# Performance work log

Measured on AMD Instinct MI355X. Metric: run time of the kernel, lower is better.

Reference implementation:

```python
import jax, jax.numpy as jnp
import numpy as np

B, M, I = 32, 8192, 256
TEMPERATURE = 1.0


def setup_inputs() -> dict:
    key = jax.random.key(0)
    k1, k2, k3, k4 = jax.random.split(key, 4)
    memory = jax.random.normal(k1, (B, M, I), dtype=jnp.float32)
    qkey = jax.random.normal(k2, (B, I), dtype=jnp.float32)
    beta = jax.random.uniform(k3, (B,), dtype=jnp.float32)
    # xavier-uniform init for Linear(I, I)
    limit = float(np.sqrt(6.0 / (I + I)))
    W = jax.random.uniform(k4, (I, I), dtype=jnp.float32, minval=-limit, maxval=limit)
    b = jnp.zeros((I,), dtype=jnp.float32)
    return {"memory": memory, "key": qkey, "beta": beta, "W": W, "b": b}


def reference(memory, key, beta, W, b):
    # projected_key = tanh(key @ W^T + b)  -- torch Linear stores weight [out, in]
    projected_key = jnp.tanh(key @ W.T + b)                      # [B, I]
    diff = projected_key[:, None, :] - memory                    # [B, M, I]
    distances = jnp.sum(diff * diff, axis=-1)                    # [B, M]
    similarity = -distances
    weights = jax.nn.softmax(beta[:, None] * similarity / TEMPERATURE, axis=-1)  # [B, M]
    read_vector = jnp.einsum('bm,bmi->bi', weights, memory)      # [B, I]
    return weights, read_vector, similarity
```

## Files before the change

### kernel.cpp

```cpp
#include <hip/hip_runtime.h>
#include <math.h>

constexpr int Bdim = 32;
constexpr int Mdim = 8192;
constexpr int Idim = 256;
constexpr int ROWS_PER_BLOCK = 128;
constexpr int ROWS_PER_WAVE = 32;
constexpr int NCHUNK = Mdim / ROWS_PER_BLOCK;
constexpr int NSLICE = 8;

__global__ void proj_key_kernel(const float* __restrict__ key,
                                const float* __restrict__ W,
                                const float* __restrict__ bias,
                                float* __restrict__ pk) {
    int b = blockIdx.x;
    int i = threadIdx.x;
    __shared__ float kq[Idim];
    kq[i] = key[b * Idim + i];
    __syncthreads();
    const float4* w4 = (const float4*)(W + (size_t)i * Idim);
    const float4* k4 = (const float4*)kq;
    float s = bias[i];
    #pragma unroll 4
    for (int k = 0; k < Idim / 4; ++k) {
        float4 wv = w4[k];
        float4 kv = k4[k];
        s += wv.x * kv.x + wv.y * kv.y + wv.z * kv.z + wv.w * kv.w;
    }
    pk[b * Idim + i] = tanhf(s);
}

__global__ void fused_pass1_kernel(const float* __restrict__ memory,
                                   const float* __restrict__ pk,
                                   const float* __restrict__ beta,
                                   float* __restrict__ sim,
                                   float* __restrict__ pvec,
                                   float* __restrict__ pmx,
                                   float* __restrict__ psum) {
    int b = blockIdx.x / NCHUNK;
    int c = blockIdx.x % NCHUNK;
    int wave = threadIdx.x >> 6;
    int lane = threadIdx.x & 63;
    float bt = beta[b];

    float4 pkv = ((const float4*)(pk + b * Idim))[lane];

    int row0 = c * ROWS_PER_BLOCK + wave * ROWS_PER_WAVE;
    const float* base = memory + ((size_t)b * Mdim + row0) * Idim;
    float* simp = sim + (size_t)b * Mdim + row0;

    float mx = -INFINITY, ssum = 0.f;
    float4 acc = make_float4(0.f, 0.f, 0.f, 0.f);
    float my_sim = 0.f;

    auto body = [&](float4 mv, int r) {
        float dx = pkv.x - mv.x, dy = pkv.y - mv.y;
        float dz = pkv.z - mv.z, dw = pkv.w - mv.w;
        float s = dx * dx + dy * dy + dz * dz + dw * dw;
        #pragma unroll
        for (int off = 32; off; off >>= 1) s += __shfl_xor(s, off, 64);
        if (lane == r) my_sim = -s;
        float a = -bt * s;
        if (a > mx) {
            float sc = __expf(mx - a);
            ssum *= sc;
            acc.x *= sc; acc.y *= sc; acc.z *= sc; acc.w *= sc;
            mx = a;
        }
        float p = __expf(a - mx);
        ssum += p;
        acc.x = fmaf(p, mv.x, acc.x);
        acc.y = fmaf(p, mv.y, acc.y);
        acc.z = fmaf(p, mv.z, acc.z);
        acc.w = fmaf(p, mv.w, acc.w);
    };

    const float4* rp = (const float4*)base + lane;
    float4 cur = rp[0];
    float4 nxt = rp[64];
    #pragma unroll 2
    for (int r = 0; r < ROWS_PER_WAVE - 2; ++r) {
        float4 pf = rp[(size_t)(r + 2) * 64];
        body(cur, r);
        cur = nxt;
        nxt = pf;
    }
    body(cur, ROWS_PER_WAVE - 2);
    body(nxt, ROWS_PER_WAVE - 1);

    if (lane < 32) simp[lane] = my_sim;

    __shared__ float lacc[4][Idim];
    __shared__ float lmx[4], lsum[4];
    ((float4*)lacc[wave])[lane] = acc;
    if (lane == 0) { lmx[wave] = mx; lsum[wave] = ssum; }
    __syncthreads();

    float MX = fmaxf(fmaxf(lmx[0], lmx[1]), fmaxf(lmx[2], lmx[3]));
    float e0 = __expf(lmx[0] - MX), e1 = __expf(lmx[1] - MX);
    float e2 = __expf(lmx[2] - MX), e3 = __expf(lmx[3] - MX);
    int i = threadIdx.x;
    float v = lacc[0][i] * e0 + lacc[1][i] * e1 + lacc[2][i] * e2 + lacc[3][i] * e3;
    size_t pc = (size_t)b * NCHUNK + c;
    pvec[pc * Idim + i] = v;
    if (threadIdx.x == 0) {
        pmx[pc] = MX;
        psum[pc] = lsum[0] * e0 + lsum[1] * e1 + lsum[2] * e2 + lsum[3] * e3;
    }
}

__global__ void epilogue_kernel(const float* __restrict__ pvec,
                                const float* __restrict__ pmx,
                                const float* __restrict__ psum,
                                const float* __restrict__ sim,
                                const float* __restrict__ beta,
                                float* __restrict__ read_vec,
                                float* __restrict__ weights) {
    int b = blockIdx.x / NSLICE;
    int slice = blockIdx.x % NSLICE;
    int tid = threadIdx.x;
    __shared__ float e[NCHUNK];
    __shared__ float MXs, sInvs;

    if (tid < NCHUNK) {
        float m = pmx[(size_t)b * NCHUNK + tid];
        float mm = m;
        #pragma unroll
        for (int off = 32; off; off >>= 1) mm = fmaxf(mm, __shfl_xor(mm, off, 64));
        float ec = __expf(m - mm);
        e[tid] = ec;
        float sc = psum[(size_t)b * NCHUNK + tid] * ec;
        #pragma unroll
        for (int off = 32; off; off >>= 1) sc += __shfl_xor(sc, off, 64);
        if (tid == 0) { MXs = mm; sInvs = 1.f / sc; }
    }
    __syncthreads();

    float MX = MXs, inv = sInvs;

    if (slice == 0) {
        float v = 0.f;
        const float* p = pvec + (size_t)b * NCHUNK * Idim + tid;
        #pragma unroll 8
        for (int c = 0; c < NCHUNK; ++c) v += p[(size_t)c * Idim] * e[c];
        read_vec[(size_t)b * Idim + tid] = v * inv;
    }

    float bt = beta[b];
    int m4 = slice * (Mdim / NSLICE / 4) + tid;
    float4 s = ((const float4*)(sim + (size_t)b * Mdim))[m4];
    float4 w;
    w.x = __expf(bt * s.x - MX) * inv;
    w.y = __expf(bt * s.y - MX) * inv;
    w.z = __expf(bt * s.z - MX) * inv;
    w.w = __expf(bt * s.w - MX) * inv;
    ((float4*)(weights + (size_t)b * Mdim))[m4] = w;
}

extern "C" void kernel_launch(void* const* d_in, const int* in_sizes, int n_in,
                              void* d_out, int out_size, void* d_ws, size_t ws_size,
                              hipStream_t stream) {
    const float* memory = (const float*)d_in[0];
    const float* key    = (const float*)d_in[1];
    const float* beta   = (const float*)d_in[2];
    const float* W      = (const float*)d_in[3];
    const float* bias   = (const float*)d_in[4];

    float* out = (float*)d_out;
    float* weights  = out;
    float* read_vec = out + (size_t)Bdim * Mdim;
    float* sim      = read_vec + (size_t)Bdim * Idim;

    float* pk   = (float*)d_ws;
    float* pvec = pk + (size_t)Bdim * Idim;
    float* pmx  = pvec + (size_t)Bdim * NCHUNK * Idim;
    float* psum = pmx + (size_t)Bdim * NCHUNK;

    proj_key_kernel<<<Bdim, Idim, 0, stream>>>(key, W, bias, pk);
    fused_pass1_kernel<<<Bdim * NCHUNK, 256, 0, stream>>>(memory, pk, beta,
                                                          sim, pvec, pmx, psum);
    epilogue_kernel<<<Bdim * NSLICE, 256, 0, stream>>>(pvec, pmx, psum, sim, beta,
                                                       read_vec, weights);
}
```

Baseline: 62.35 us.

## Batch eight rows per online-softmax step and split projection across more blocks

The main pass now loads eight memory rows at once, does their eight butterfly reductions interleaved, and updates the running max once per group instead of once per row. This exposes more memory-level and shuffle-level parallelism and cuts serial rescale branches. The projection kernel is also split over 8x more blocks, with 8 lanes cooperating on each output row via shuffles, so it uses more of the GPU. Register pressure rises from holding eight float4 rows.

```diff
diff --git a/kernel.cpp b/kernel.cpp
--- a/kernel.cpp
+++ b/kernel.cpp
@@ -13,21 +13,25 @@
                                 const float* __restrict__ W,
                                 const float* __restrict__ bias,
                                 float* __restrict__ pk) {
-    int b = blockIdx.x;
-    int i = threadIdx.x;
-    __shared__ float kq[Idim];
-    kq[i] = key[b * Idim + i];
-    __syncthreads();
-    const float4* w4 = (const float4*)(W + (size_t)i * Idim);
-    const float4* k4 = (const float4*)kq;
-    float s = bias[i];
-    #pragma unroll 4
-    for (int k = 0; k < Idim / 4; ++k) {
+    int b = blockIdx.x >> 3;
+    int slice = blockIdx.x & 7;
+    int tid = threadIdx.x;
+    int row = slice * 32 + (tid >> 3);
+    int seg = tid & 7;
+
+    const float4* w4 = (const float4*)(W + (size_t)row * Idim) + seg * 8;
+    const float4* k4 = (const float4*)(key + (size_t)b * Idim) + seg * 8;
+    float s = 0.f;
+    #pragma unroll
+    for (int k = 0; k < 8; ++k) {
         float4 wv = w4[k];
         float4 kv = k4[k];
         s += wv.x * kv.x + wv.y * kv.y + wv.z * kv.z + wv.w * kv.w;
     }
-    pk[b * Idim + i] = tanhf(s);
+    s += __shfl_xor(s, 4, 64);
+    s += __shfl_xor(s, 2, 64);
+    s += __shfl_xor(s, 1, 64);
+    if (seg == 0) pk[(size_t)b * Idim + row] = tanhf(s + bias[row]);
 }
 
 __global__ void fused_pass1_kernel(const float* __restrict__ memory,
@@ -43,7 +47,7 @@
     int lane = threadIdx.x & 63;
     float bt = beta[b];
 
-    float4 pkv = ((const float4*)(pk + b * Idim))[lane];
+    float4 pkv = ((const float4*)(pk + (size_t)b * Idim))[lane];
 
     int row0 = c * ROWS_PER_BLOCK + wave * ROWS_PER_WAVE;
     const float* base = memory + ((size_t)b * Mdim + row0) * Idim;
@@ -53,41 +57,50 @@
     float4 acc = make_float4(0.f, 0.f, 0.f, 0.f);
     float my_sim = 0.f;
 
-    auto body = [&](float4 mv, int r) {
-        float dx = pkv.x - mv.x, dy = pkv.y - mv.y;
-        float dz = pkv.z - mv.z, dw = pkv.w - mv.w;
-        float s = dx * dx + dy * dy + dz * dz + dw * dw;
+    const float4* rp = (const float4*)base + lane;
+
+    for (int g = 0; g < ROWS_PER_WAVE / 8; ++g) {
+        float4 m[8];
         #pragma unroll
-        for (int off = 32; off; off >>= 1) s += __shfl_xor(s, off, 64);
-        if (lane == r) my_sim = -s;
-        float a = -bt * s;
-        if (a > mx) {
-            float sc = __expf(mx - a);
+        for (int j = 0; j < 8; ++j)
+            m[j] = rp[(size_t)(g * 8 + j) * 64];
+
+        float s[8];
+        #pragma unroll
+        for (int j = 0; j < 8; ++j) {
+            float dx = pkv.x - m[j].x, dy = pkv.y - m[j].y;
+            float dz = pkv.z - m[j].z, dw = pkv.w - m[j].w;
+            s[j] = dx * dx + dy * dy + dz * dz + dw * dw;
+        }
+        #pragma unroll
+        for (int off = 32; off; off >>= 1) {
+            #pragma unroll
+            for (int j = 0; j < 8; ++j) s[j] += __shfl_xor(s[j], off, 64);
+        }
+        if ((lane >> 3) == g) my_sim = -s[lane & 7];
+
+        #pragma unroll
+        for (int j = 0; j < 8; ++j) s[j] = -bt * s[j];
+        float gm = fmaxf(fmaxf(fmaxf(s[0], s[1]), fmaxf(s[2], s[3])),
+                         fmaxf(fmaxf(s[4], s[5]), fmaxf(s[6], s[7])));
+        if (gm > mx) {
+            float sc = __expf(mx - gm);
             ssum *= sc;
             acc.x *= sc; acc.y *= sc; acc.z *= sc; acc.w *= sc;
-            mx = a;
+            mx = gm;
         }
-        float p = __expf(a - mx);
-        ssum += p;
-        acc.x = fmaf(p, mv.x, acc.x);
-        acc.y = fmaf(p, mv.y, acc.y);
-        acc.z = fmaf(p, mv.z, acc.z);
-        acc.w = fmaf(p, mv.w, acc.w);
-    };
-
-    const float4* rp = (const float4*)base + lane;
-    float4 cur = rp[0];
-    float4 nxt = rp[64];
-    #pragma unroll 2
-    for (int r = 0; r < ROWS_PER_WAVE - 2; ++r) {
-        float4 pf = rp[(size_t)(r + 2) * 64];
-        body(cur, r);
-        cur = nxt;
-        nxt = pf;
+        float ps = 0.f;
+        #pragma unroll
+        for (int j = 0; j < 8; ++j) {
+            float p = __expf(s[j] - mx);
+            ps += p;
+            acc.x = fmaf(p, m[j].x, acc.x);
+            acc.y = fmaf(p, m[j].y, acc.y);
+            acc.z = fmaf(p, m[j].z, acc.z);
+            acc.w = fmaf(p, m[j].w, acc.w);
+        }
+        ssum += ps;
     }
-    body(cur, ROWS_PER_WAVE - 2);
-    body(nxt, ROWS_PER_WAVE - 1);
-
     if (lane < 32) simp[lane] = my_sim;
 
     __shared__ float lacc[4][Idim];
@@ -176,7 +189,7 @@
     float* pmx  = pvec + (size_t)Bdim * NCHUNK * Idim;
     float* psum = pmx + (size_t)Bdim * NCHUNK;
 
-    proj_key_kernel<<<Bdim, Idim, 0, stream>>>(key, W, bias, pk);
+    proj_key_kernel<<<Bdim * 8, 256, 0, stream>>>(key, W, bias, pk);
     fused_pass1_kernel<<<Bdim * NCHUNK, 256, 0, stream>>>(memory, pk, beta,
                                                           sim, pvec, pmx, psum);
     epilogue_kernel<<<Bdim * NSLICE, 256, 0, stream>>>(pvec, pmx, psum, sim, beta,
```

Result: faster. 53.90 us (median of 2 runs) (-13.6%).
